# Optimization experiments

Hardware: AMD Instinct MI355X
Metric: run time of the kernel (lower is better)

## Reference

```python
import jax, jax.numpy as jnp
import numpy as np

DIM = 512
HEADS = 8
HEAD_DIM = DIM // HEADS
EPS = 1e-6
LN_EPS = 1e-5


def setup_inputs() -> dict:
    key = jax.random.key(0)
    ks = jax.random.split(key, 7)
    B, S = 2, 2048
    std = 1.0 / np.sqrt(DIM)
    return {
        "x": jax.random.normal(ks[0], (B, S, DIM), dtype=jnp.float32),
        "Wq": jax.random.normal(ks[1], (DIM, DIM), dtype=jnp.float32) * std,
        "Wk": jax.random.normal(ks[2], (DIM, DIM), dtype=jnp.float32) * std,
        "Wv": jax.random.normal(ks[3], (DIM, DIM), dtype=jnp.float32) * std,
        "Wo": jax.random.normal(ks[4], (DIM, DIM), dtype=jnp.float32) * std,
        "ln_gamma": jnp.ones((DIM,), dtype=jnp.float32),
        "ln_beta": jnp.zeros((DIM,), dtype=jnp.float32),
    }


def _hardsigmoid(x):
    return jnp.clip(x / 6.0 + 0.5, 0.0, 1.0)


def _softshrink(x, lambd=0.5):
    return jnp.where(x > lambd, x - lambd, jnp.where(x < -lambd, x + lambd, 0.0))


def reference(x, Wq, Wk, Wv, Wo, ln_gamma, ln_beta):
    B, S, D = x.shape
    # torch Linear: y = x @ W.T
    q = (x @ Wq.T).reshape(B, S, HEADS, HEAD_DIM).transpose(0, 2, 1, 3)
    k = (x @ Wk.T).reshape(B, S, HEADS, HEAD_DIM).transpose(0, 2, 1, 3)
    v = (x @ Wv.T).reshape(B, S, HEADS, HEAD_DIM).transpose(0, 2, 1, 3)
    scale = 1.0 / np.sqrt(HEAD_DIM)
    scores = jnp.einsum("bhqd,bhkd->bhqk", q, k) * scale  # [B,H,S,S]
    attn_soft = jax.nn.softmax(scores, axis=-1)
    gated = attn_soft * _hardsigmoid(scores)
    attn_weights = gated / (gated.sum(axis=-1, keepdims=True) + EPS)
    attn_out = jnp.einsum("bhqk,bhkd->bhqd", attn_weights, v)
    attn_out = attn_out.transpose(0, 2, 1, 3).reshape(B, S, D)
    out = attn_out @ Wo.T
    out = out / (1.0 + jnp.abs(out))  # softsign
    out = out + _softshrink(x)
    # LayerNorm over last dim
    mu = out.mean(axis=-1, keepdims=True)
    var = ((out - mu) ** 2).mean(axis=-1, keepdims=True)
    out = (out - mu) * jax.lax.rsqrt(var + LN_EPS) * ln_gamma + ln_beta
    return out
```

## Files before the change

### kernel.cpp

```cpp
#include <hip/hip_runtime.h>

#define DIMD 512
#define NB 2
#define SEQ 2048
#define NHEADS 8
#define HDIM 64
#define MROWS (NB*SEQ)

typedef short s16x8 __attribute__((ext_vector_type(8)));
typedef float f32x4 __attribute__((ext_vector_type(4)));
typedef float f32x16 __attribute__((ext_vector_type(16)));
typedef unsigned short u16;
typedef unsigned int u32;

__device__ __forceinline__ u16 f2bf(float f) {
    union { float f; u32 u; } c; c.f = f;
    u32 u = c.u;
    return (u16)((u + 0x7FFFu + ((u >> 16) & 1u)) >> 16);
}
__device__ __forceinline__ float bf2f(u16 v) {
    union { u32 u; float f; } c; c.u = ((u32)v) << 16;
    return c.f;
}

__device__ __forceinline__ f32x4 mfma16(s16x8 a, s16x8 b, f32x4 c) {
    return __builtin_amdgcn_mfma_f32_16x16x32_bf16(a, b, c, 0, 0, 0);
}
__device__ __forceinline__ f32x16 mfma32(s16x8 a, s16x8 b, f32x16 c) {
    return __builtin_amdgcn_mfma_f32_32x32x16_bf16(a, b, c, 0, 0, 0);
}

#define GLDS16(g, l) __builtin_amdgcn_global_load_lds( \
    (const __attribute__((address_space(1))) void*)(g), \
    (__attribute__((address_space(3))) void*)(l), 16, 0, 0)

#define ESCF 0.180336880111f
#define HSC2 0.115524530f

__global__ void cvt_all(const float* __restrict__ x, const float* __restrict__ Wq,
                        const float* __restrict__ Wk, const float* __restrict__ Wv,
                        const float* __restrict__ Wo,
                        u16* __restrict__ xb, u16* __restrict__ wqkv, u16* __restrict__ wo) {
    int i = blockIdx.x * blockDim.x + threadIdx.x;
    const float* src; u16* dst; int idx;
    if (i < 524288) { src = x; dst = xb; idx = i; }
    else {
        int jj = i - 524288;
        int which = jj >> 16; idx = jj & 65535;
        src = which == 0 ? Wq : which == 1 ? Wk : which == 2 ? Wv : Wo;
        dst = which < 3 ? wqkv + which*DIMD*DIMD : wo;
    }
    float4 v = reinterpret_cast<const float4*>(src)[idx];
    ushort4 o;
    o.x = f2bf(v.x); o.y = f2bf(v.y); o.z = f2bf(v.z); o.w = f2bf(v.w);
    reinterpret_cast<ushort4*>(dst)[idx] = o;
}

template<int WMODE>
__global__ __launch_bounds__(256) void gemm128(const u16* __restrict__ A, const u16* __restrict__ Bm,
                                               void* __restrict__ Cout, void* __restrict__ Cout2,
                                               void* __restrict__ Cout3, int M, int N, int K) {
    __shared__ u16 As[128*64];
    __shared__ u16 Bs[128*64];
    const int bm0 = blockIdx.x * 128, bn0 = blockIdx.y * 128;
    const int t = threadIdx.x;
    const int w = t >> 6, l = t & 63;
    const int lg = l >> 4, lr = l & 15;
    const int wm = w >> 1, wn = w & 1;
    f32x4 acc[4][4] = {};
    const int srow = w*32 + (l >> 3);
    const int swc = ((l & 7) ^ ((l >> 3) & 7)) * 8;
    const u16* asrc = A  + (size_t)(bm0 + srow)*K + swc;
    const u16* bsrc = Bm + (size_t)(bn0 + srow)*K + swc;
    const int ldsb = w*2048;

    for (int k0 = 0; k0 < K; k0 += 64) {
        #pragma unroll
        for (int g = 0; g < 4; g++) {
            GLDS16(asrc + (size_t)g*8*K + k0, &As[ldsb + g*512]);
            GLDS16(bsrc + (size_t)g*8*K + k0, &Bs[ldsb + g*512]);
        }
        __syncthreads();
        #pragma unroll
        for (int ks = 0; ks < 2; ks++) {
            const int swr = ((ks*4 + lg) ^ (lr & 7)) * 8;
            s16x8 af[4], bfr[4];
            #pragma unroll
            for (int fm = 0; fm < 4; fm++)
                af[fm] = *(const s16x8*)&As[(wm*64 + fm*16 + lr)*64 + swr];
            #pragma unroll
            for (int fn = 0; fn < 4; fn++)
                bfr[fn] = *(const s16x8*)&Bs[(wn*64 + fn*16 + lr)*64 + swr];
            #pragma unroll
            for (int fm = 0; fm < 4; fm++)
                #pragma unroll
                for (int fn = 0; fn < 4; fn++)
                    acc[fm][fn] = mfma16(af[fm], bfr[fn], acc[fm][fn]);
        }
        __syncthreads();
    }

    const int region = (WMODE == 3) ? (bn0 >> 9) : 0;
    const float qsc = (WMODE == 3 && region == 0) ? ESCF : 1.0f;
    #pragma unroll
    for (int fm = 0; fm < 4; fm++) {
        #pragma unroll
        for (int fn = 0; fn < 4; fn++) {
            const int mb = bm0 + wm*64 + fm*16 + lg*4;
            const int n  = bn0 + wn*64 + fn*16 + lr;
            if (WMODE == 2) {
                float* C = (float*)Cout;
                #pragma unroll
                for (int i = 0; i < 4; i++)
                    C[(size_t)(mb + i)*N + n] = acc[fm][fn][i];
            } else {
                const int nl = n & 511;
                if (region == 2) {
                    const int b = mb >> 11, s0 = mb & 2047;
                    const int h = nl >> 6, d = nl & 63;
                    ushort4 pk;
                    pk.x = f2bf(acc[fm][fn][0]);
                    pk.y = f2bf(acc[fm][fn][1]);
                    pk.z = f2bf(acc[fm][fn][2]);
                    pk.w = f2bf(acc[fm][fn][3]);
                    *(ushort4*)((u16*)Cout3 + (size_t)((b*8 + h)*64 + d)*2048 + s0) = pk;
                } else {
                    u16* C = region == 0 ? (u16*)Cout : (u16*)Cout2;
                    #pragma unroll
                    for (int i = 0; i < 4; i++)
                        C[(size_t)(mb + i)*512 + nl] = f2bf(acc[fm][fn][i] * qsc);
                }
            }
        }
    }
}

__global__ __launch_bounds__(256) void gemm_bt2(const u16* __restrict__ A, const u16* __restrict__ Bm,
                                                u16* __restrict__ Cout, int M, int N, int K) {
    __shared__ u16 As[64*64];
    __shared__ u16 Bs[64*64];
    const int bm0 = blockIdx.x * 64, bn0 = blockIdx.y * 64;
    const int t = threadIdx.x;
    const int w = t >> 6, l = t & 63;
    const int lg = l >> 4, lr = l & 15;
    const int wm = w >> 1, wn = w & 1;
    f32x4 acc[2][2] = {};
    const int srow = t >> 3;
    const int scol = (t & 7) * 8;

    for (int k0 = 0; k0 < K; k0 += 64) {
        #pragma unroll
        for (int c = 0; c < 2; c++) {
            const u16* ga = A  + (size_t)(bm0 + c*32 + srow)*K + k0 + scol;
            const u16* gb = Bm + (size_t)(bn0 + c*32 + srow)*K + k0 + scol;
            GLDS16(ga, (char*)As + c*4096 + w*1024);
            GLDS16(gb, (char*)Bs + c*4096 + w*1024);
        }
        __syncthreads();
        #pragma unroll
        for (int ks = 0; ks < 2; ks++) {
            s16x8 af[2], bfr[2];
            #pragma unroll
            for (int fm = 0; fm < 2; fm++)
                af[fm] = *(const s16x8*)&As[(wm*32 + fm*16 + lr)*64 + ks*32 + lg*8];
            #pragma unroll
            for (int fn = 0; fn < 2; fn++)
                bfr[fn] = *(const s16x8*)&Bs[(wn*32 + fn*16 + lr)*64 + ks*32 + lg*8];
            #pragma unroll
            for (int fm = 0; fm < 2; fm++)
                #pragma unroll
                for (int fn = 0; fn < 2; fn++)
                    acc[fm][fn] = mfma16(af[fm], bfr[fn], acc[fm][fn]);
        }
        __syncthreads();
    }

    #pragma unroll
    for (int fm = 0; fm < 2; fm++)
        #pragma unroll
        for (int fn = 0; fn < 2; fn++) {
            const int mb = bm0 + wm*32 + fm*16 + lg*4;
            const int n  = bn0 + wn*32 + fn*16 + lr;
            #pragma unroll
            for (int i = 0; i < 4; i++)
                Cout[(size_t)(mb + i)*N + n] = f2bf(acc[fm][fn][i]);
        }
}

__device__ __forceinline__ void attn_phase64(const u16* Kc, const u16* Vc, const s16x8* qf,
                                             f32x16& o0, f32x16& o1, float& gacc,
                                             int ln, int hi, int l7) {
    #pragma unroll
    for (int kb = 0; kb < 2; kb++) {
        f32x16 sc = {};
        __builtin_amdgcn_s_setprio(1);
        #pragma unroll
        for (int c = 0; c < 4; c++) {
            s16x8 kf = *(const s16x8*)&Kc[(kb*32 + ln)*64 + (((c << 1) | hi) ^ l7)*8];
            sc = mfma32(kf, qf[c], sc);
        }
        __builtin_amdgcn_s_setprio(0);
        u32 u[4][2];
        #pragma unroll
        for (int b2 = 0; b2 < 4; b2++) {
            float ww[4];
            #pragma unroll
            for (int r = 0; r < 4; r++) {
                const float s = sc[b2*4 + r];
                const float e = exp2f(s);
                const float hs = __builtin_amdgcn_fmed3f(s*HSC2 + 0.5f, 0.f, 1.f);
                ww[r] = e*hs;
            }
            gacc += (ww[0] + ww[1]) + (ww[2] + ww[3]);
            asm("v_cvt_pk_bf16_f32 %0, %1, %2" : "=v"(u[b2][0]) : "v"(ww[0]), "v"(ww[1]));
            asm("v_cvt_pk_bf16_f32 %0, %1, %2" : "=v"(u[b2][1]) : "v"(ww[2]), "v"(ww[3]));
        }
        #pragma unroll
        for (int c16 = 0; c16 < 2; c16++) {
            u32 x0 = u[2*c16][0], y0 = u[2*c16+1][0];
            u32 x1 = u[2*c16][1], y1 = u[2*c16+1][1];
            asm("v_permlane32_swap_b32 %0, %1" : "+v"(x0), "+v"(y0));
            asm("v_permlane32_swap_b32 %0, %1" : "+v"(x1), "+v"(y1));
            union { u32 uu[4]; s16x8 v; } pa;
            pa.uu[0] = x0; pa.uu[1] = x1; pa.uu[2] = y0; pa.uu[3] = y1;
            const int ccv = kb*4 + c16*2 + hi;
            s16x8 vf0 = *(const s16x8*)&Vc[(size_t)ln*64        + (ccv ^ l7)*8];
            s16x8 vf1 = *(const s16x8*)&Vc[(size_t)(32 + ln)*64 + (ccv ^ l7)*8];
            __builtin_amdgcn_s_setprio(1);
            o0 = mfma32(pa.v, vf0, o0);
            o1 = mfma32(pa.v, vf1, o1);
            __builtin_amdgcn_s_setprio(0);
        }
    }
}

__global__ __launch_bounds__(256) void attn_split(const u16* __restrict__ q, const u16* __restrict__ k,
                                                  const u16* __restrict__ vt,
                                                  u16* __restrict__ opart, float* __restrict__ gpart) {
    __shared__ u16 Ks[2][64*64];
    __shared__ u16 Vs[2][64*64];
    const int bid = blockIdx.x;
    const int xcd = bid & 7, j = bid >> 3;
    const int g8 = j >> 4, qt = j & 15;
    const int bhks = xcd*8 + g8;
    const int bh = bhks >> 2, ks = bhks & 3;
    const int b = bh >> 3, h = bh & 7;
    const int qb0 = qt * 128;
    const int t = threadIdx.x;
    const int w = t >> 6, l = t & 63;
    const int ln = l & 31, hi = l >> 5, l7 = l & 7;

    const size_t qrow = (size_t)(b*SEQ + qb0 + w*32 + ln);
    s16x8 qf[4];
    #pragma unroll
    for (int c = 0; c < 4; c++)
        qf[c] = *(const s16x8*)(q + qrow*DIMD + h*HDIM + c*16 + hi*8);

    const int sr = l >> 3;
    const int swc = ((l & 7) ^ sr) * 8;
    const u16* ksrc = k  + (size_t)(b*SEQ + ks*512 + w*16 + sr)*DIMD + h*HDIM + swc;
    const u16* vsrc = vt + (size_t)bh*HDIM*SEQ + (size_t)(w*16 + sr)*SEQ + ks*512 + swc;
    const int ldsw = w*1024;

    f32x16 o0 = {}, o1 = {};
    float gacc = 0.f;

    #pragma unroll
    for (int g = 0; g < 2; g++) {
        GLDS16(ksrc + (size_t)g*8*DIMD, &Ks[0][ldsw + g*512]);
        GLDS16(vsrc + (size_t)g*8*SEQ,  &Vs[0][ldsw + g*512]);
    }
    __syncthreads();

    #pragma unroll 1
    for (int tp = 0; tp < 4; ++tp) {
        const int tt0 = tp*2;
        {
            const int adv = (tt0 + 1) * 64;
            #pragma unroll
            for (int g = 0; g < 2; g++) {
                GLDS16(ksrc + (size_t)(adv)*DIMD + (size_t)g*8*DIMD, &Ks[1][ldsw + g*512]);
                GLDS16(vsrc + (size_t)g*8*SEQ + adv,                 &Vs[1][ldsw + g*512]);
            }
        }
        attn_phase64(&Ks[0][0], &Vs[0][0], qf, o0, o1, gacc, ln, hi, l7);
        __syncthreads();
        if (tp < 3) {
            const int adv = (tt0 + 2) * 64;
            #pragma unroll
            for (int g = 0; g < 2; g++) {
                GLDS16(ksrc + (size_t)(adv)*DIMD + (size_t)g*8*DIMD, &Ks[0][ldsw + g*512]);
                GLDS16(vsrc + (size_t)g*8*SEQ + adv,                 &Vs[0][ldsw + g*512]);
            }
        }
        attn_phase64(&Ks[1][0], &Vs[1][0], qf, o0, o1, gacc, ln, hi, l7);
        __syncthreads();
    }

    gacc += __shfl_xor(gacc, 32);
    if (l < 32)
        gpart[((size_t)ks*16 + bh)*SEQ + qb0 + w*32 + l] = gacc;

    u16* op = opart + ((size_t)ks*MROWS + b*SEQ + qb0 + w*32)*DIMD + h*HDIM;
    #pragma unroll
    for (int i = 0; i < 16; i++) {
        const int qr = (i & 3) + 8*(i >> 2) + 4*hi;
        op[(size_t)qr*DIMD + ln]      = f2bf(o0[i]);
        op[(size_t)qr*DIMD + 32 + ln] = f2bf(o1[i]);
    }
}

__global__ __launch_bounds__(256) void attn_combine(const u16* __restrict__ opart,
                                                    const float* __restrict__ gpart,
                                                    u16* __restrict__ attn) {
    const int idx = blockIdx.x*256 + threadIdx.x;
    const int row = idx >> 6;
    const int colb = (idx & 63) * 8;
    const int b = row >> 11, s = row & 2047, h = colb >> 6;
    float g = 0.f;
    #pragma unroll
    for (int p = 0; p < 4; p++)
        g += gpart[((size_t)p*16 + b*8 + h)*SEQ + s];
    const float inv = 1.f / g;
    float acc[8] = {};
    #pragma unroll
    for (int p = 0; p < 4; p++) {
        s16x8 v = *(const s16x8*)(opart + ((size_t)p*MROWS + row)*DIMD + colb);
        #pragma unroll
        for (int j2 = 0; j2 < 8; j2++) acc[j2] += bf2f((u16)v[j2]);
    }
    union { u16 r[8]; s16x8 v; } o;
    #pragma unroll
    for (int j2 = 0; j2 < 8; j2++) o.r[j2] = f2bf(acc[j2]*inv);
    *(s16x8*)(attn + (size_t)row*DIMD + colb) = o.v;
}

__global__ __launch_bounds__(256) void ln_epilogue(const u16* __restrict__ proj, const float* __restrict__ x,
                                                   const float* __restrict__ gamma, const float* __restrict__ beta,
                                                   float* __restrict__ out) {
    const int row = blockIdx.x*4 + (threadIdx.x >> 6);
    const int l = threadIdx.x & 63;
    const u16* pr = proj + (size_t)row*DIMD + l*8;
    const float* xr = x  + (size_t)row*DIMD + l*8;
    s16x8 pv = *(const s16x8*)pr;
    float tv[8];
    float s = 0.f, s2 = 0.f;
    #pragma unroll
    for (int j = 0; j < 2; j++) {
        float4 xv = *(const float4*)(xr + j*4);
        float xa[4] = {xv.x, xv.y, xv.z, xv.w};
        #pragma unroll
        for (int qq = 0; qq < 4; qq++) {
            const float p = bf2f((u16)pv[j*4+qq]);
            const float ss = p / (1.f + fabsf(p));
            const float xx = xa[qq];
            const float sh = xx > 0.5f ? xx - 0.5f : (xx < -0.5f ? xx + 0.5f : 0.f);
            const float tt = ss + sh;
            tv[j*4+qq] = tt; s += tt; s2 += tt*tt;
        }
    }
    #pragma unroll
    for (int m = 1; m < 64; m <<= 1) { s += __shfl_xor(s, m); s2 += __shfl_xor(s2, m); }
    const float mu = s * (1.f/512.f);
    float var = s2 * (1.f/512.f) - mu*mu;
    const float rstd = rsqrtf(var + 1e-5f);
    #pragma unroll
    for (int j = 0; j < 2; j++) {
        float4 g  = *(const float4*)(gamma + l*8 + j*4);
        float4 bb = *(const float4*)(beta  + l*8 + j*4);
        float4 ov;
        ov.x = (tv[j*4+0]-mu)*rstd*g.x + bb.x;
        ov.y = (tv[j*4+1]-mu)*rstd*g.y + bb.y;
        ov.z = (tv[j*4+2]-mu)*rstd*g.z + bb.z;
        ov.w = (tv[j*4+3]-mu)*rstd*g.w + bb.w;
        *(float4*)(out + (size_t)row*DIMD + l*8 + j*4) = ov;
    }
}

extern "C" void kernel_launch(void* const* d_in, const int* in_sizes, int n_in,
                              void* d_out, int out_size, void* d_ws, size_t ws_size,
                              hipStream_t stream) {
    const float* x     = (const float*)d_in[0];
    const float* Wq    = (const float*)d_in[1];
    const float* Wk    = (const float*)d_in[2];
    const float* Wv    = (const float*)d_in[3];
    const float* Wo    = (const float*)d_in[4];
    const float* gamma = (const float*)d_in[5];
    const float* beta  = (const float*)d_in[6];
    float* out = (float*)d_out;
    char* ws = (char*)d_ws;

    u16* xb    = (u16*)(ws);
    u16* wqkvb = (u16*)(ws + (4<<20));
    u16* wob   = (u16*)(ws + (4<<20) + (1536<<10));
    u16* qb    = (u16*)(ws + (6<<20));
    u16* kb    = (u16*)(ws + (10<<20));
    u16* vtb   = (u16*)(ws + (14<<20));
    u16* ab    = (u16*)(ws + (18<<20));
    u16* proj  = (u16*)(ws + (22<<20));
    u16* opart = (u16*)(ws + (26<<20));
    float* gpart = (float*)(ws + (42<<20));

    cvt_all<<<3072, 256, 0, stream>>>(x, Wq, Wk, Wv, Wo, xb, wqkvb, wob);

    gemm128<3><<<dim3(MROWS/128, 1536/128), 256, 0, stream>>>(xb, wqkvb, qb, kb, vtb, MROWS, 1536, DIMD);

    attn_split<<<1024, 256, 0, stream>>>(qb, kb, vtb, opart, gpart);
    attn_combine<<<1024, 256, 0, stream>>>(opart, gpart, ab);

    gemm_bt2<<<dim3(MROWS/64, DIMD/64), 256, 0, stream>>>(ab, wob, proj, MROWS, DIMD, DIMD);

    ln_epilogue<<<MROWS/4, 256, 0, stream>>>(proj, x, gamma, beta, out);
}
```

Before: 76.42 us.

## Software-pipeline attention split: overlap QK^T of next tile with softmax-PV of current

Replaces the double-buffered loop with a fully unrolled, hand-scheduled pipeline. K is staged through three LDS buffers and V through two, and the QK^T MFMAs for tile t+1 are issued before the softmax/PV work of tile t. Synchronisation uses explicit vmcnt waits plus s_barrier instead of __syncthreads, and exp2f is replaced with a raw v_exp_f32 instruction. The aim is to hide exp/VALU latency behind MFMA work and cut barrier stalls. In exchange it holds more score registers live, uses more LDS, and the hand-written buffer indexing is fragile.

Measured after the change: 69.54 us. 9.0% less time.

```diff
diff --git a/kernel.cpp b/kernel.cpp
--- a/kernel.cpp
+++ b/kernel.cpp
@@ -28,6 +28,9 @@
 }
 __device__ __forceinline__ f32x16 mfma32(s16x8 a, s16x8 b, f32x16 c) {
     return __builtin_amdgcn_mfma_f32_32x32x16_bf16(a, b, c, 0, 0, 0);
+}
+__device__ __forceinline__ float fexp2(float x) {
+    float r; asm("v_exp_f32 %0, %1" : "=v"(r) : "v"(x)); return r;
 }
 
 #define GLDS16(g, l) __builtin_amdgcn_global_load_lds( \
@@ -187,57 +190,10 @@
         }
 }
 
-__device__ __forceinline__ void attn_phase64(const u16* Kc, const u16* Vc, const s16x8* qf,
-                                             f32x16& o0, f32x16& o1, float& gacc,
-                                             int ln, int hi, int l7) {
-    #pragma unroll
-    for (int kb = 0; kb < 2; kb++) {
-        f32x16 sc = {};
-        __builtin_amdgcn_s_setprio(1);
-        #pragma unroll
-        for (int c = 0; c < 4; c++) {
-            s16x8 kf = *(const s16x8*)&Kc[(kb*32 + ln)*64 + (((c << 1) | hi) ^ l7)*8];
-            sc = mfma32(kf, qf[c], sc);
-        }
-        __builtin_amdgcn_s_setprio(0);
-        u32 u[4][2];
-        #pragma unroll
-        for (int b2 = 0; b2 < 4; b2++) {
-            float ww[4];
-            #pragma unroll
-            for (int r = 0; r < 4; r++) {
-                const float s = sc[b2*4 + r];
-                const float e = exp2f(s);
-                const float hs = __builtin_amdgcn_fmed3f(s*HSC2 + 0.5f, 0.f, 1.f);
-                ww[r] = e*hs;
-            }
-            gacc += (ww[0] + ww[1]) + (ww[2] + ww[3]);
-            asm("v_cvt_pk_bf16_f32 %0, %1, %2" : "=v"(u[b2][0]) : "v"(ww[0]), "v"(ww[1]));
-            asm("v_cvt_pk_bf16_f32 %0, %1, %2" : "=v"(u[b2][1]) : "v"(ww[2]), "v"(ww[3]));
-        }
-        #pragma unroll
-        for (int c16 = 0; c16 < 2; c16++) {
-            u32 x0 = u[2*c16][0], y0 = u[2*c16+1][0];
-            u32 x1 = u[2*c16][1], y1 = u[2*c16+1][1];
-            asm("v_permlane32_swap_b32 %0, %1" : "+v"(x0), "+v"(y0));
-            asm("v_permlane32_swap_b32 %0, %1" : "+v"(x1), "+v"(y1));
-            union { u32 uu[4]; s16x8 v; } pa;
-            pa.uu[0] = x0; pa.uu[1] = x1; pa.uu[2] = y0; pa.uu[3] = y1;
-            const int ccv = kb*4 + c16*2 + hi;
-            s16x8 vf0 = *(const s16x8*)&Vc[(size_t)ln*64        + (ccv ^ l7)*8];
-            s16x8 vf1 = *(const s16x8*)&Vc[(size_t)(32 + ln)*64 + (ccv ^ l7)*8];
-            __builtin_amdgcn_s_setprio(1);
-            o0 = mfma32(pa.v, vf0, o0);
-            o1 = mfma32(pa.v, vf1, o1);
-            __builtin_amdgcn_s_setprio(0);
-        }
-    }
-}
-
 __global__ __launch_bounds__(256) void attn_split(const u16* __restrict__ q, const u16* __restrict__ k,
                                                   const u16* __restrict__ vt,
                                                   u16* __restrict__ opart, float* __restrict__ gpart) {
-    __shared__ u16 Ks[2][64*64];
+    __shared__ u16 Ks[3][64*64];
     __shared__ u16 Vs[2][64*64];
     const int bid = blockIdx.x;
     const int xcd = bid & 7, j = bid >> 3;
@@ -265,37 +221,73 @@
     f32x16 o0 = {}, o1 = {};
     float gacc = 0.f;
 
-    #pragma unroll
-    for (int g = 0; g < 2; g++) {
-        GLDS16(ksrc + (size_t)g*8*DIMD, &Ks[0][ldsw + g*512]);
-        GLDS16(vsrc + (size_t)g*8*SEQ,  &Vs[0][ldsw + g*512]);
-    }
-    __syncthreads();
-
-    #pragma unroll 1
-    for (int tp = 0; tp < 4; ++tp) {
-        const int tt0 = tp*2;
-        {
-            const int adv = (tt0 + 1) * 64;
-            #pragma unroll
-            for (int g = 0; g < 2; g++) {
-                GLDS16(ksrc + (size_t)(adv)*DIMD + (size_t)g*8*DIMD, &Ks[1][ldsw + g*512]);
-                GLDS16(vsrc + (size_t)g*8*SEQ + adv,                 &Vs[1][ldsw + g*512]);
-            }
-        }
-        attn_phase64(&Ks[0][0], &Vs[0][0], qf, o0, o1, gacc, ln, hi, l7);
-        __syncthreads();
-        if (tp < 3) {
-            const int adv = (tt0 + 2) * 64;
-            #pragma unroll
-            for (int g = 0; g < 2; g++) {
-                GLDS16(ksrc + (size_t)(adv)*DIMD + (size_t)g*8*DIMD, &Ks[0][ldsw + g*512]);
-                GLDS16(vsrc + (size_t)g*8*SEQ + adv,                 &Vs[0][ldsw + g*512]);
-            }
-        }
-        attn_phase64(&Ks[1][0], &Vs[1][0], qf, o0, o1, gacc, ln, hi, l7);
-        __syncthreads();
-    }
+#define SV(T, B) do { GLDS16(vsrc + (T)*64,                 &Vs[B][ldsw]); \
+                      GLDS16(vsrc + (size_t)8*SEQ + (T)*64, &Vs[B][ldsw + 512]); } while(0)
+#define SK(T, B) do { GLDS16(ksrc + (size_t)((T)*64)*DIMD,     &Ks[B][ldsw]); \
+                      GLDS16(ksrc + (size_t)((T)*64 + 8)*DIMD, &Ks[B][ldsw + 512]); } while(0)
+#define WB(N) do { asm volatile("s_waitcnt vmcnt(" #N ")" ::: "memory"); \
+                   __builtin_amdgcn_s_barrier(); \
+                   asm volatile("" ::: "memory"); } while(0)
+#define QKH(B, KB, SC) do { SC = (f32x16){}; \
+    __builtin_amdgcn_s_setprio(1); \
+    _Pragma("unroll") for (int c_ = 0; c_ < 4; c_++) { \
+        const int ch_ = (((c_ << 1) | hi) ^ l7) * 8; \
+        s16x8 kf_ = *(const s16x8*)&Ks[B][((KB)*32 + ln)*64 + ch_]; \
+        SC = mfma32(kf_, qf[c_], SC); } \
+    __builtin_amdgcn_s_setprio(0); } while(0)
+#define SMPV(SC, KB, VB) do { \
+    u32 up_[4][2]; \
+    _Pragma("unroll") for (int b2_ = 0; b2_ < 4; b2_++) { \
+        const float s0_ = SC[b2_*4+0], s1_ = SC[b2_*4+1]; \
+        const float s2_ = SC[b2_*4+2], s3_ = SC[b2_*4+3]; \
+        const float w0_ = fexp2(s0_) * __builtin_amdgcn_fmed3f(s0_*HSC2 + 0.5f, 0.f, 1.f); \
+        const float w1_ = fexp2(s1_) * __builtin_amdgcn_fmed3f(s1_*HSC2 + 0.5f, 0.f, 1.f); \
+        const float w2_ = fexp2(s2_) * __builtin_amdgcn_fmed3f(s2_*HSC2 + 0.5f, 0.f, 1.f); \
+        const float w3_ = fexp2(s3_) * __builtin_amdgcn_fmed3f(s3_*HSC2 + 0.5f, 0.f, 1.f); \
+        gacc += (w0_ + w1_) + (w2_ + w3_); \
+        asm("v_cvt_pk_bf16_f32 %0, %1, %2" : "=v"(up_[b2_][0]) : "v"(w0_), "v"(w1_)); \
+        asm("v_cvt_pk_bf16_f32 %0, %1, %2" : "=v"(up_[b2_][1]) : "v"(w2_), "v"(w3_)); } \
+    _Pragma("unroll") for (int c16_ = 0; c16_ < 2; c16_++) { \
+        u32 x0_ = up_[2*c16_][0], y0_ = up_[2*c16_+1][0]; \
+        u32 x1_ = up_[2*c16_][1], y1_ = up_[2*c16_+1][1]; \
+        asm("v_permlane32_swap_b32 %0, %1" : "+v"(x0_), "+v"(y0_)); \
+        asm("v_permlane32_swap_b32 %0, %1" : "+v"(x1_), "+v"(y1_)); \
+        union { u32 w[4]; s16x8 v; } pa_; \
+        pa_.w[0] = x0_; pa_.w[1] = x1_; pa_.w[2] = y0_; pa_.w[3] = y1_; \
+        const int ccv_ = (KB)*4 + c16_*2 + hi; \
+        s16x8 vf0_ = *(const s16x8*)&Vs[VB][(size_t)ln*64        + (ccv_ ^ l7)*8]; \
+        s16x8 vf1_ = *(const s16x8*)&Vs[VB][(size_t)(32 + ln)*64 + (ccv_ ^ l7)*8]; \
+        __builtin_amdgcn_s_setprio(1); \
+        o0 = mfma32(pa_.v, vf0_, o0); \
+        o1 = mfma32(pa_.v, vf1_, o1); \
+        __builtin_amdgcn_s_setprio(0); } } while(0)
+
+    f32x16 a0, a1, b0, b1;
+    SV(0,0); SK(0,0); SK(1,1);
+    WB(2);
+    QKH(0,0,a0); SK(2,2); QKH(0,1,a1);
+    WB(2);
+    SV(1,1); QKH(1,0,b0); SK(3,0); SMPV(a0,0,0); QKH(1,1,b1); SMPV(a1,1,0);
+    WB(2);
+    SV(2,0); QKH(2,0,a0); SK(4,1); SMPV(b0,0,1); QKH(2,1,a1); SMPV(b1,1,1);
+    WB(2);
+    SV(3,1); QKH(0,0,b0); SK(5,2); SMPV(a0,0,0); QKH(0,1,b1); SMPV(a1,1,0);
+    WB(2);
+    SV(4,0); QKH(1,0,a0); SK(6,0); SMPV(b0,0,1); QKH(1,1,a1); SMPV(b1,1,1);
+    WB(2);
+    SV(5,1); QKH(2,0,b0); SK(7,1); SMPV(a0,0,0); QKH(2,1,b1); SMPV(a1,1,0);
+    WB(2);
+    SV(6,0); QKH(0,0,a0); SMPV(b0,0,1); QKH(0,1,a1); SMPV(b1,1,1);
+    WB(0);
+    SV(7,1); QKH(1,0,b0); SMPV(a0,0,0); QKH(1,1,b1); SMPV(a1,1,0);
+    WB(0);
+    SMPV(b0,0,1); SMPV(b1,1,1);
+
+#undef SV
+#undef SK
+#undef WB
+#undef QKH
+#undef SMPV
 
     gacc += __shfl_xor(gacc, 32);
     if (l < 32)
```
